# Kernel optimization log

Hardware: AMD Instinct MI355X
Metric: run time of the kernel (lower is better)

## Reference

```python
import jax, jax.numpy as jnp
import numpy as np

V, D, H, O = 50257, 256, 256, 10
L, N = 2048, 64


def setup_inputs() -> dict:
    key = jax.random.key(0)
    ks = jax.random.split(key, 20)
    s = 0.05
    p = {
        'x': jax.random.randint(ks[0], (L, N), 0, V, dtype=jnp.int64) if jax.config.jax_enable_x64 else jax.random.randint(ks[0], (L, N), 0, V, dtype=jnp.int32),
        'emb': jax.random.normal(ks[1], (V, D), jnp.float32) * s,
        'Wii': jax.random.normal(ks[2], (H, D), jnp.float32) * s, 'bii': jnp.zeros((H,), jnp.float32),
        'Whi': jax.random.normal(ks[3], (H, H), jnp.float32) * s, 'bhi': jnp.zeros((H,), jnp.float32),
        'Wif': jax.random.normal(ks[4], (H, D), jnp.float32) * s, 'bif': jnp.zeros((H,), jnp.float32),
        'Whf': jax.random.normal(ks[5], (H, H), jnp.float32) * s, 'bhf': jnp.zeros((H,), jnp.float32),
        'Wig': jax.random.normal(ks[6], (H, D), jnp.float32) * s, 'big': jnp.zeros((H,), jnp.float32),
        'Whg': jax.random.normal(ks[7], (H, H), jnp.float32) * s, 'bhg': jnp.zeros((H,), jnp.float32),
        'Wio': jax.random.normal(ks[8], (H, D), jnp.float32) * s, 'bio': jnp.zeros((H,), jnp.float32),
        'Who': jax.random.normal(ks[9], (H, H), jnp.float32) * s, 'bho': jnp.zeros((H,), jnp.float32),
        'Wout': jax.random.normal(ks[10], (O, H), jnp.float32) * s, 'bout': jnp.zeros((O,), jnp.float32),
    }
    return p


def _lstm_last_h(xe, Wii, bii, Whi, bhi, Wif, bif, Whf, bhf,
                 Wig, big, Whg, bhg, Wio, bio, Who, bho):
    # xe: [L, N, D]. Precompute all input-side gate projections in one big GEMM-like pass.
    xi = jnp.einsum('lnd,hd->lnh', xe, Wii) + bii
    xf = jnp.einsum('lnd,hd->lnh', xe, Wif) + bif
    xg = jnp.einsum('lnd,hd->lnh', xe, Wig) + big
    xo = jnp.einsum('lnd,hd->lnh', xe, Wio) + bio

    n = xe.shape[1]
    h0 = jnp.zeros((n, Whi.shape[0]), xe.dtype)
    c0 = jnp.zeros((n, Whi.shape[0]), xe.dtype)

    def step(carry, gates):
        h, c = carry
        gi, gf, gg, go = gates
        it = jax.nn.sigmoid(gi + h @ Whi.T + bhi)
        ft = jax.nn.sigmoid(gf + h @ Whf.T + bhf)
        gt = jnp.tanh(gg + h @ Whg.T + bhg)
        ot = jax.nn.sigmoid(go + h @ Who.T + bho)
        ct = ft * c + it * gt
        ht = ot * jnp.tanh(ct)
        return (ht, ct), None

    (hT, _), _ = jax.lax.scan(step, (h0, c0), (xi, xf, xg, xo))
    return hT  # [N, H]


def reference(x, emb, Wii, bii, Whi, bhi, Wif, bif, Whf, bhf,
              Wig, big, Whg, bhg, Wio, bio, Who, bho, Wout, bout):
    # EmbeddingBag with bag size 1 and mode='mean' == plain embedding lookup
    xe = emb[x]  # [L, N, D]
    hT = _lstm_last_h(xe, Wii, bii, Whi, bhi, Wif, bif, Whf, bhf,
                      Wig, big, Whg, bhg, Wio, bio, Who, bho)
    return hT @ Wout.T + bout  # [N, O]
```

## Files before the change

kernel.cpp:

```cpp
#include <hip/hip_runtime.h>


using half_t  = _Float16;
using half2_t = __attribute__((ext_vector_type(2))) _Float16;
using half8_t = __attribute__((ext_vector_type(8))) _Float16;
using f32x4   = __attribute__((ext_vector_type(4))) float;

#define L_SEQ   2048
#define CHUNK_L 1024
#define NB      64
#define DIM     256
#define P4      1024
#define CM      (CHUNK_L * NB)

#define OFF_GATES 0ull
#define SZ_GATES  ((unsigned long long)CM * P4 * 2)
#define OFF_EMBH  (OFF_GATES + SZ_GATES)
#define SZ_EMBH   (50257ull * 256 * 2)
#define OFF_WX    (OFF_EMBH + SZ_EMBH)
#define SZ_WX     (1024ull * 256 * 2)
#define OFF_WH    (OFF_WX + SZ_WX)
#define SZ_WH     (1024ull * 256 * 2)
#define OFF_B4    (OFF_WH + SZ_WH)
#define SZ_B4     (1024ull * 4)
#define OFF_ST    (OFF_B4 + SZ_B4)
#define SZ_ST     (2ull * NB * DIM * 4)
#define WS_NEED   (OFF_ST + SZ_ST)

__device__ __forceinline__ float sigm(float x) {
  x = fminf(fmaxf(x, -30.f), 30.f);
  return 1.f / (1.f + __expf(-x));
}
__device__ __forceinline__ float tanh_(float x) {
  x = fminf(fmaxf(x, -15.f), 15.f);
  float t = __expf(2.f * x);
  return (t - 1.f) / (t + 1.f);
}
__device__ __forceinline__ float dot8(half8_t w, half8_t h, float acc) {
  acc = __builtin_amdgcn_fdot2((half2_t)__builtin_shufflevector(w, w, 0, 1),
                               (half2_t)__builtin_shufflevector(h, h, 0, 1), acc, false);
  acc = __builtin_amdgcn_fdot2((half2_t)__builtin_shufflevector(w, w, 2, 3),
                               (half2_t)__builtin_shufflevector(h, h, 2, 3), acc, false);
  acc = __builtin_amdgcn_fdot2((half2_t)__builtin_shufflevector(w, w, 4, 5),
                               (half2_t)__builtin_shufflevector(h, h, 4, 5), acc, false);
  acc = __builtin_amdgcn_fdot2((half2_t)__builtin_shufflevector(w, w, 6, 7),
                               (half2_t)__builtin_shufflevector(h, h, 6, 7), acc, false);
  return acc;
}

__global__ void ws_too_small_kernel(float* out, float sz) {
  if (threadIdx.x == 0 && blockIdx.x == 0) out[0] = sz;
}

__global__ void cvt_emb_kernel(const float* __restrict__ src, half_t* __restrict__ dst,
                               int total8) {
  int i = blockIdx.x * blockDim.x + threadIdx.x;
  if (i >= total8) return;
  const float4* s = (const float4*)src + (size_t)i * 2;
  float4 a = s[0], b = s[1];
  half8_t o;
  o[0] = (half_t)a.x; o[1] = (half_t)a.y; o[2] = (half_t)a.z; o[3] = (half_t)a.w;
  o[4] = (half_t)b.x; o[5] = (half_t)b.y; o[6] = (half_t)b.z; o[7] = (half_t)b.w;
  *((half8_t*)dst + i) = o;
}

__global__ void pack_w_kernel(const float* __restrict__ Wii, const float* __restrict__ Whi,
                              const float* __restrict__ Wif, const float* __restrict__ Whf,
                              const float* __restrict__ Wig, const float* __restrict__ Whg,
                              const float* __restrict__ Wio, const float* __restrict__ Who,
                              const float* __restrict__ bii, const float* __restrict__ bhi,
                              const float* __restrict__ bif, const float* __restrict__ bhf,
                              const float* __restrict__ big_, const float* __restrict__ bhg,
                              const float* __restrict__ bio, const float* __restrict__ bho,
                              half_t* __restrict__ Wx4h, half_t* __restrict__ Wh4c,
                              float* __restrict__ b4) {
  int p = blockIdx.x;
  int k = threadIdx.x;
  int g = p >> 8, h = p & 255;
  const float* Wx = g == 0 ? Wii : g == 1 ? Wif : g == 2 ? Wig : Wio;
  const float* Wh = g == 0 ? Whi : g == 1 ? Whf : g == 2 ? Whg : Who;
  Wx4h[(size_t)p * DIM + k] = (half_t)Wx[h * DIM + k];
  Wh4c[((size_t)(k >> 3) * P4 + p) * 8 + (k & 7)] = (half_t)Wh[h * DIM + k];
  if (k == 0) {
    const float* bx = g == 0 ? bii : g == 1 ? bif : g == 2 ? big_ : bio;
    const float* bh = g == 0 ? bhi : g == 1 ? bhf : g == 2 ? bhg : bho;
    b4[p] = bx[h] + bh[h];
  }
}

#define BK   32
#define LSTR 40
__global__ __launch_bounds__(256) void gemm_gates_kernel(
    const half_t* __restrict__ embh, const int* __restrict__ xc,
    const half_t* __restrict__ Wx4h, const float* __restrict__ b4,
    half_t* __restrict__ gates) {
  __shared__ __align__(16) half_t As[128 * LSTR];
  __shared__ __align__(16) half_t Ws[128 * LSTR];
  const int tid  = threadIdx.x;
  const int lane = tid & 63;
  const int wave = tid >> 6;
  const int wm = wave >> 1, wn = wave & 1;
  const int M0 = blockIdx.x * 128;
  const int P0 = blockIdx.y * 128;
  const int r0 = tid >> 2, s0 = tid & 3;

  const size_t arow0 = (size_t)xc[M0 + r0] * DIM;
  const size_t arow1 = (size_t)xc[M0 + 64 + r0] * DIM;
  const size_t wrow0 = (size_t)(P0 + r0) * DIM;
  const size_t wrow1 = (size_t)(P0 + 64 + r0) * DIM;

  f32x4 acc[4][4] = {};
  const int fr = lane & 15;
  const int kq = lane >> 4;

  for (int kt = 0; kt < 8; ++kt) {
    const int k0 = kt * BK;
    half8_t a0 = *(const half8_t*)(embh + arow0 + k0 + s0 * 8);
    half8_t a1 = *(const half8_t*)(embh + arow1 + k0 + s0 * 8);
    half8_t w0 = *(const half8_t*)(Wx4h + wrow0 + k0 + s0 * 8);
    half8_t w1 = *(const half8_t*)(Wx4h + wrow1 + k0 + s0 * 8);
    __syncthreads();
    *(half8_t*)(As + r0 * LSTR + s0 * 8)        = a0;
    *(half8_t*)(As + (r0 + 64) * LSTR + s0 * 8) = a1;
    *(half8_t*)(Ws + r0 * LSTR + s0 * 8)        = w0;
    *(half8_t*)(Ws + (r0 + 64) * LSTR + s0 * 8) = w1;
    __syncthreads();
    half8_t af[4], bf[4];
#pragma unroll
    for (int mi = 0; mi < 4; ++mi)
      af[mi] = *(const half8_t*)(As + (wm * 64 + mi * 16 + fr) * LSTR + kq * 8);
#pragma unroll
    for (int ni = 0; ni < 4; ++ni)
      bf[ni] = *(const half8_t*)(Ws + (wn * 64 + ni * 16 + fr) * LSTR + kq * 8);
#pragma unroll
    for (int mi = 0; mi < 4; ++mi)
#pragma unroll
      for (int ni = 0; ni < 4; ++ni)
        acc[mi][ni] = __builtin_amdgcn_mfma_f32_16x16x32_f16(af[mi], bf[ni], acc[mi][ni], 0, 0, 0);
  }
  const int rbase = (lane >> 4) * 4;
#pragma unroll
  for (int ni = 0; ni < 4; ++ni) {
    const int p = P0 + wn * 64 + ni * 16 + fr;
    const float bias = b4[p];
#pragma unroll
    for (int mi = 0; mi < 4; ++mi) {
      const int m = M0 + wm * 64 + mi * 16 + rbase;
#pragma unroll
      for (int r = 0; r < 4; ++r)
        gates[(size_t)(m + r) * P4 + p] = (half_t)(acc[mi][ni][r] + bias);
    }
  }
}

__global__ __launch_bounds__(512, 2) void lstm_kernel(
    const half_t* __restrict__ gates, const half_t* __restrict__ Wh4c,
    const float* __restrict__ Wout, const float* __restrict__ bout,
    float* __restrict__ out, float* __restrict__ state,
    int first, int last) {
  const int n   = blockIdx.x;
  const int tid = threadIdx.x;
  const int j   = tid & 255;
  const int kh  = tid >> 8;
  __shared__ __align__(16) half_t wlds[8][P4][8];
  __shared__ __align__(16) half_t hbuf[2][DIM];
  __shared__ __align__(16) float  partial4[DIM][4];
  __shared__ float hfin[DIM];

  const half8_t* W8 = (const half8_t*)Wh4c;
  for (int i = tid; i < 8192; i += 512) {
    const int slot = i >> 10, p = i & 1023;
    const int kc = (slot >> 2) * 16 + 12 + (slot & 3);
    *(half8_t*)wlds[slot][p] = W8[kc * P4 + p];
  }
  const int kc0 = kh * 16;
  const int b0 = j, b1 = 256 + j, b2 = 512 + j, b3 = 768 + j;
  half8_t wreg[12][4];
#pragma unroll
  for (int kc = 0; kc < 12; ++kc) {
    wreg[kc][0] = W8[(kc0 + kc) * P4 + b0];
    wreg[kc][1] = W8[(kc0 + kc) * P4 + b1];
    wreg[kc][2] = W8[(kc0 + kc) * P4 + b2];
    wreg[kc][3] = W8[(kc0 + kc) * P4 + b3];
  }
#pragma unroll
  for (int kc = 0; kc < 12; ++kc)
#pragma unroll
    for (int g = 0; g < 4; ++g)
      asm volatile("" : "+v"(wreg[kc][g]));

  float c = 0.f, hkeep = 0.f;
  if (kh == 0) {
    float h0 = 0.f;
    if (!first) { h0 = state[n * DIM + j]; c = state[NB * DIM + n * DIM + j]; }
    hbuf[0][j] = (half_t)h0;
    hkeep = h0;
  }
  const half_t* gbase = gates + (size_t)n * P4;
  float g0 = 0.f, g1 = 0.f, g2 = 0.f, g3 = 0.f;
  if (kh == 1) {
    g0 = (float)gbase[b0]; g1 = (float)gbase[b1];
    g2 = (float)gbase[b2]; g3 = (float)gbase[b3];
  }
  __syncthreads();

#pragma unroll 1
  for (int l = 0; l < CHUNK_L; ++l) {
    float a0 = 0.f, a1 = 0.f, a2 = 0.f, a3 = 0.f;
    half_t ng0, ng1, ng2, ng3;
    if (kh == 1) {
      a0 = g0; a1 = g1; a2 = g2; a3 = g3;
      const half_t* gp2 = gbase + (size_t)(l + 1) * NB * P4;
      ng0 = gp2[b0]; ng1 = gp2[b1]; ng2 = gp2[b2]; ng3 = gp2[b3];
    }
    const half8_t* hp = (const half8_t*)hbuf[l & 1] + kc0;
#pragma unroll
    for (int kc = 0; kc < 12; ++kc) {
      const half8_t h8 = hp[kc];
      a0 = dot8(wreg[kc][0], h8, a0);
      a1 = dot8(wreg[kc][1], h8, a1);
      a2 = dot8(wreg[kc][2], h8, a2);
      a3 = dot8(wreg[kc][3], h8, a3);
    }
#pragma unroll
    for (int s = 0; s < 4; ++s) {
      const half8_t h8 = hp[12 + s];
      const int slot = kh * 4 + s;
      a0 = dot8(*(const half8_t*)wlds[slot][b0], h8, a0);
      a1 = dot8(*(const half8_t*)wlds[slot][b1], h8, a1);
      a2 = dot8(*(const half8_t*)wlds[slot][b2], h8, a2);
      a3 = dot8(*(const half8_t*)wlds[slot][b3], h8, a3);
    }
    if (kh == 1) {
      float4 pv; pv.x = a0; pv.y = a1; pv.z = a2; pv.w = a3;
      *(float4*)partial4[j] = pv;
      g0 = (float)ng0; g1 = (float)ng1; g2 = (float)ng2; g3 = (float)ng3;
    }
    __syncthreads();
    if (kh == 0) {
      float4 pv = *(const float4*)partial4[j];
      a0 += pv.x; a1 += pv.y; a2 += pv.z; a3 += pv.w;
      const float it = sigm(a0), ft = sigm(a1), gt = tanh_(a2), ot = sigm(a3);
      c = ft * c + it * gt;
      const float h = ot * tanh_(c);
      hbuf[(l + 1) & 1][j] = (half_t)h;
      hkeep = h;
    }
    __syncthreads();
  }
  if (kh == 0) {
    if (!last) { state[n * DIM + j] = hkeep; state[NB * DIM + n * DIM + j] = c; }
    hfin[j] = hkeep;
  }
  __syncthreads();
  if (last && tid < 10) {
    float s = bout[tid];
    const float* wrow = Wout + tid * DIM;
#pragma unroll 4
    for (int k = 0; k < DIM; ++k) s += hfin[k] * wrow[k];
    out[n * 10 + tid] = s;
  }
}

extern "C" void kernel_launch(void* const* d_in, const int* in_sizes, int n_in,
                              void* d_out, int out_size, void* d_ws, size_t ws_size,
                              hipStream_t stream) {
  const int*   x    = (const int*)d_in[0];
  const float* emb  = (const float*)d_in[1];
  const float* Wii  = (const float*)d_in[2];  const float* bii = (const float*)d_in[3];
  const float* Whi  = (const float*)d_in[4];  const float* bhi = (const float*)d_in[5];
  const float* Wif  = (const float*)d_in[6];  const float* bif = (const float*)d_in[7];
  const float* Whf  = (const float*)d_in[8];  const float* bhf = (const float*)d_in[9];
  const float* Wig  = (const float*)d_in[10]; const float* big_ = (const float*)d_in[11];
  const float* Whg  = (const float*)d_in[12]; const float* bhg = (const float*)d_in[13];
  const float* Wio  = (const float*)d_in[14]; const float* bio = (const float*)d_in[15];
  const float* Who  = (const float*)d_in[16]; const float* bho = (const float*)d_in[17];
  const float* Wout = (const float*)d_in[18]; const float* bout = (const float*)d_in[19];
  float* out = (float*)d_out;

  if (ws_size < WS_NEED) {
    hipLaunchKernelGGL(ws_too_small_kernel, dim3(1), dim3(64), 0, stream, out, (float)ws_size);
    return;
  }
  char* ws = (char*)d_ws;
  half_t* gates = (half_t*)(ws + OFF_GATES);
  half_t* embh  = (half_t*)(ws + OFF_EMBH);
  half_t* Wx4h  = (half_t*)(ws + OFF_WX);
  half_t* Wh4c  = (half_t*)(ws + OFF_WH);
  float*  b4    = (float*)(ws + OFF_B4);
  float*  state = (float*)(ws + OFF_ST);

  const int total8 = 50257 * 32;
  hipLaunchKernelGGL(cvt_emb_kernel, dim3((total8 + 255) / 256), dim3(256), 0, stream,
                     emb, embh, total8);
  hipLaunchKernelGGL(pack_w_kernel, dim3(1024), dim3(256), 0, stream,
                     Wii, Whi, Wif, Whf, Wig, Whg, Wio, Who,
                     bii, bhi, bif, bhf, big_, bhg, bio, bho,
                     Wx4h, Wh4c, b4);
  hipLaunchKernelGGL(gemm_gates_kernel, dim3(CM / 128, P4 / 128), dim3(256), 0, stream,
                     embh, x, Wx4h, b4, gates);
  hipLaunchKernelGGL(lstm_kernel, dim3(NB), dim3(512), 0, stream,
                     gates, Wh4c, Wout, bout, out, state, 1, 0);
  hipLaunchKernelGGL(gemm_gates_kernel, dim3(CM / 128, P4 / 128), dim3(256), 0, stream,
                     embh, x + (size_t)CHUNK_L * NB, Wx4h, b4, gates);
  hipLaunchKernelGGL(lstm_kernel, dim3(NB), dim3(512), 0, stream,
                     gates, Wh4c, Wout, bout, out, state, 0, 1);
}
```

Before: 3.241 ms.

## Stream part of recurrent weights from global memory each step instead of register-pinning

The recurrent weight split changes. Each thread now pins 4 chunks in registers, reads 4 chunks from LDS, and streams 8 chunks from global/L2 every timestep through a rotating double buffer of 8 half8 registers, where previously it pinned 12. Barriers are replaced with explicit sched_barrier + waitcnt + s_barrier, which keeps global loads outstanding across the barrier, and the launch-bounds occupancy hint of 2 is dropped. The aim is to relieve register pressure and hide the streamed-load latency behind the dot products. The cost is extra L2 traffic on the latency-critical sequential loop.

```diff
diff --git a/kernel.cpp b/kernel.cpp
--- a/kernel.cpp
+++ b/kernel.cpp
@@ -47,6 +47,13 @@
                                (half2_t)__builtin_shufflevector(h, h, 6, 7), acc, false);
   return acc;
 }
+
+#define SBAR() do {                                   \
+    __builtin_amdgcn_sched_barrier(0);                \
+    asm volatile("s_waitcnt lgkmcnt(0)" ::);          \
+    __builtin_amdgcn_s_barrier();                     \
+    __builtin_amdgcn_sched_barrier(0);                \
+  } while (0)
 
 __global__ void ws_too_small_kernel(float* out, float sz) {
   if (threadIdx.x == 0 && blockIdx.x == 0) out[0] = sz;
@@ -153,11 +160,36 @@
   }
 }
 
-__global__ __launch_bounds__(512, 2) void lstm_kernel(
-    const half_t* __restrict__ gates, const half_t* __restrict__ Wh4c,
-    const float* __restrict__ Wout, const float* __restrict__ bout,
-    float* __restrict__ out, float* __restrict__ state,
-    int first, int last) {
+#define DECLR(r) half8_t R##r##_0, R##r##_1, R##r##_2, R##r##_3;
+#define LOADR(r)                                   \
+  R##r##_0 = W8[(kcb + (r)) * P4 + p0];            \
+  R##r##_1 = W8[(kcb + (r)) * P4 + p1];            \
+  R##r##_2 = W8[(kcb + (r)) * P4 + p2];            \
+  R##r##_3 = W8[(kcb + (r)) * P4 + p3];
+#define PINR(r)                                                             \
+  asm volatile("" : "+v"(R##r##_0), "+v"(R##r##_1), "+v"(R##r##_2),         \
+                    "+v"(R##r##_3));
+#define RGRP(r) { const half8_t hh = hp[r];        \
+  a0 = dot8(R##r##_0, hh, a0); a1 = dot8(R##r##_1, hh, a1);                 \
+  a2 = dot8(R##r##_2, hh, a2); a3 = dot8(R##r##_3, hh, a3); }
+
+#define LGRP(r) { const half8_t hh = hp[r]; const int sl = (kh << 2) + (r) - 4; \
+  a0 = dot8(*(const half8_t*)wlds[sl][p0], hh, a0);                         \
+  a1 = dot8(*(const half8_t*)wlds[sl][p1], hh, a1);                         \
+  a2 = dot8(*(const half8_t*)wlds[sl][p2], hh, a2);                         \
+  a3 = dot8(*(const half8_t*)wlds[sl][p3], hh, a3); }
+
+#define SGRP(r, sa, sb, sc, sd, rn) { const half8_t hh = hp[r];             \
+  a0 = dot8(sa, hh, a0); sa = W8[(kcb + (rn)) * P4 + p0];                   \
+  a1 = dot8(sb, hh, a1); sb = W8[(kcb + (rn)) * P4 + p1];                   \
+  a2 = dot8(sc, hh, a2); sc = W8[(kcb + (rn)) * P4 + p2];                   \
+  a3 = dot8(sd, hh, a3); sd = W8[(kcb + (rn)) * P4 + p3]; }
+
+__global__ __launch_bounds__(512)
+void lstm_kernel(const half_t* __restrict__ gates, const half_t* __restrict__ Wh4c,
+                 const float* __restrict__ Wout, const float* __restrict__ bout,
+                 float* __restrict__ out, float* __restrict__ state,
+                 int first, int last) {
   const int n   = blockIdx.x;
   const int tid = threadIdx.x;
   const int j   = tid & 255;
@@ -169,87 +201,76 @@
 
   const half8_t* W8 = (const half8_t*)Wh4c;
   for (int i = tid; i < 8192; i += 512) {
-    const int slot = i >> 10, p = i & 1023;
-    const int kc = (slot >> 2) * 16 + 12 + (slot & 3);
-    *(half8_t*)wlds[slot][p] = W8[kc * P4 + p];
-  }
-  const int kc0 = kh * 16;
-  const int b0 = j, b1 = 256 + j, b2 = 512 + j, b3 = 768 + j;
-  half8_t wreg[12][4];
-#pragma unroll
-  for (int kc = 0; kc < 12; ++kc) {
-    wreg[kc][0] = W8[(kc0 + kc) * P4 + b0];
-    wreg[kc][1] = W8[(kc0 + kc) * P4 + b1];
-    wreg[kc][2] = W8[(kc0 + kc) * P4 + b2];
-    wreg[kc][3] = W8[(kc0 + kc) * P4 + b3];
-  }
-#pragma unroll
-  for (int kc = 0; kc < 12; ++kc)
-#pragma unroll
-    for (int g = 0; g < 4; ++g)
-      asm volatile("" : "+v"(wreg[kc][g]));
-
-  float c = 0.f, hkeep = 0.f;
+    const int s = i >> 10, pp = i & 1023;
+    const int kc = ((s >> 2) << 4) + 4 + (s & 3);
+    *(half8_t*)wlds[s][pp] = W8[kc * P4 + pp];
+  }
+  const int kcb = kh << 4;
+  const int p0 = j, p1 = 256 + j, p2 = 512 + j, p3 = 768 + j;
+
+  DECLR(0) DECLR(1) DECLR(2) DECLR(3)
+  LOADR(0) LOADR(1) LOADR(2) LOADR(3)
+  PINR(0) PINR(1) PINR(2) PINR(3)
+  half8_t S0 = W8[(kcb + 8) * P4 + p0], S1 = W8[(kcb + 8) * P4 + p1];
+  half8_t S2 = W8[(kcb + 8) * P4 + p2], S3 = W8[(kcb + 8) * P4 + p3];
+  half8_t S4 = W8[(kcb + 9) * P4 + p0], S5 = W8[(kcb + 9) * P4 + p1];
+  half8_t S6 = W8[(kcb + 9) * P4 + p2], S7 = W8[(kcb + 9) * P4 + p3];
+
+  float cc = 0.f, hkeep = 0.f;
   if (kh == 0) {
     float h0 = 0.f;
-    if (!first) { h0 = state[n * DIM + j]; c = state[NB * DIM + n * DIM + j]; }
+    if (!first) { h0 = state[n * DIM + j]; cc = state[NB * DIM + n * DIM + j]; }
     hbuf[0][j] = (half_t)h0;
     hkeep = h0;
   }
   const half_t* gbase = gates + (size_t)n * P4;
-  float g0 = 0.f, g1 = 0.f, g2 = 0.f, g3 = 0.f;
+  float g0f = 0.f, g1f = 0.f, g2f = 0.f, g3f = 0.f;
   if (kh == 1) {
-    g0 = (float)gbase[b0]; g1 = (float)gbase[b1];
-    g2 = (float)gbase[b2]; g3 = (float)gbase[b3];
+    g0f = (float)gbase[p0]; g1f = (float)gbase[p1];
+    g2f = (float)gbase[p2]; g3f = (float)gbase[p3];
   }
   __syncthreads();
 
 #pragma unroll 1
   for (int l = 0; l < CHUNK_L; ++l) {
     float a0 = 0.f, a1 = 0.f, a2 = 0.f, a3 = 0.f;
-    half_t ng0, ng1, ng2, ng3;
+    half_t ng0 = (half_t)0.f, ng1 = ng0, ng2 = ng0, ng3 = ng0;
     if (kh == 1) {
-      a0 = g0; a1 = g1; a2 = g2; a3 = g3;
-      const half_t* gp2 = gbase + (size_t)(l + 1) * NB * P4;
-      ng0 = gp2[b0]; ng1 = gp2[b1]; ng2 = gp2[b2]; ng3 = gp2[b3];
-    }
-    const half8_t* hp = (const half8_t*)hbuf[l & 1] + kc0;
-#pragma unroll
-    for (int kc = 0; kc < 12; ++kc) {
-      const half8_t h8 = hp[kc];
-      a0 = dot8(wreg[kc][0], h8, a0);
-      a1 = dot8(wreg[kc][1], h8, a1);
-      a2 = dot8(wreg[kc][2], h8, a2);
-      a3 = dot8(wreg[kc][3], h8, a3);
-    }
-#pragma unroll
-    for (int s = 0; s < 4; ++s) {
-      const half8_t h8 = hp[12 + s];
-      const int slot = kh * 4 + s;
-      a0 = dot8(*(const half8_t*)wlds[slot][b0], h8, a0);
-      a1 = dot8(*(const half8_t*)wlds[slot][b1], h8, a1);
-      a2 = dot8(*(const half8_t*)wlds[slot][b2], h8, a2);
-      a3 = dot8(*(const half8_t*)wlds[slot][b3], h8, a3);
-    }
+      a0 = g0f; a1 = g1f; a2 = g2f; a3 = g3f;
+      const half_t* gp2 = gbase + (size_t)(l + 1) * (NB * P4);
+      ng0 = gp2[p0]; ng1 = gp2[p1]; ng2 = gp2[p2]; ng3 = gp2[p3];
+    }
+    const half8_t* hp = (const half8_t*)hbuf[l & 1] + kcb;
+    SGRP(8,  S0, S1, S2, S3, 10) LGRP(4)
+    SGRP(9,  S4, S5, S6, S7, 11) LGRP(5)
+    SGRP(10, S0, S1, S2, S3, 12) LGRP(6)
+    SGRP(11, S4, S5, S6, S7, 13) LGRP(7)
+    SGRP(12, S0, S1, S2, S3, 14) RGRP(0)
+    SGRP(13, S4, S5, S6, S7, 15) RGRP(1)
+    SGRP(14, S0, S1, S2, S3, 8)  RGRP(2)
+    SGRP(15, S4, S5, S6, S7, 9)  RGRP(3)
     if (kh == 1) {
       float4 pv; pv.x = a0; pv.y = a1; pv.z = a2; pv.w = a3;
       *(float4*)partial4[j] = pv;
-      g0 = (float)ng0; g1 = (float)ng1; g2 = (float)ng2; g3 = (float)ng3;
-    }
-    __syncthreads();
+    }
+    SBAR();
     if (kh == 0) {
       float4 pv = *(const float4*)partial4[j];
       a0 += pv.x; a1 += pv.y; a2 += pv.z; a3 += pv.w;
       const float it = sigm(a0), ft = sigm(a1), gt = tanh_(a2), ot = sigm(a3);
-      c = ft * c + it * gt;
-      const float h = ot * tanh_(c);
+      cc = ft * cc + it * gt;
+      const float h = ot * tanh_(cc);
       hbuf[(l + 1) & 1][j] = (half_t)h;
       hkeep = h;
     }
-    __syncthreads();
-  }
+    SBAR();
+    if (kh == 1) {
+      g0f = (float)ng0; g1f = (float)ng1; g2f = (float)ng2; g3f = (float)ng3;
+    }
+  }
+  __syncthreads();
   if (kh == 0) {
-    if (!last) { state[n * DIM + j] = hkeep; state[NB * DIM + n * DIM + j] = c; }
+    if (!last) { state[n * DIM + j] = hkeep; state[NB * DIM + n * DIM + j] = cc; }
     hfin[j] = hkeep;
   }
   __syncthreads();
```

Result: slower. 4.567 ms (+40.9%).
